# Kernel optimization log

Hardware: AMD Instinct MI355X
Metric: run time of the kernel (lower is better)

Reference implementation:

```python
import jax, jax.numpy as jnp
import numpy as np

MUL = 1024
DIMS = [3, 5, 7, 9]          # irrep dims for l=1,2,3,4
BN_EPS = 1e-5                # e3nn BatchNorm eps
ACT_EPS = 1e-8               # numerical guard for norm-activation sqrt
INV_SQRT_MUL = 1.0 / np.sqrt(MUL)


def bn_act(f, w):
    """e3nn BatchNorm (training mode, component normalization, mean reduce)
    followed by NormActivation(sigmoid, normalize=True).
    f: [B, mul, d] one irrep block; w: [mul] affine batchnorm weight."""
    # norm-based batchnorm: second moment per multiplicity channel
    var = jnp.mean(jnp.mean(f * f, axis=-1), axis=0)            # [mul]
    f = f * ((var + BN_EPS) ** -0.5 * w)[None, :, None]
    # norm-gated sigmoid: out = f * sigmoid(||f||) / ||f||
    n = jnp.sqrt(jnp.sum(f * f, axis=-1, keepdims=True) + ACT_EPS)  # [B, mul, 1]
    return f * (jax.nn.sigmoid(n) / n)


def setup_inputs() -> dict:
    key = jax.random.key(0)
    k = jax.random.split(key, 4)
    B = 1024
    x = jax.random.normal(k[0], (B, 2, 3, 1), dtype=jnp.float32)
    w1 = jax.random.normal(k[1], (2, MUL), dtype=jnp.float32)
    W = jax.random.normal(k[2], (5, 4, MUL, MUL), dtype=jnp.float32)
    bn_w = jnp.ones((6, 4, MUL), dtype=jnp.float32)
    w_out = jax.random.normal(k[3], (MUL, 1), dtype=jnp.float32)
    return {"x": x, "w1": w1, "W": W, "bn_w": bn_w, "w_out": w_out}


def reference(x, w1, W, bn_w, w_out):
    B = x.shape[0]
    x = x.reshape(B, 2, 3)  # '2x1e'
    # block1: only the l=1 path exists; l=2,3,4 outputs are zero
    f1 = jnp.einsum('bui,uv->bvi', x, w1) * (1.0 / jnp.sqrt(2.0).astype(x.dtype))
    fields = [bn_act(f1, bn_w[0, 0])]
    for i, d in enumerate(DIMS[1:]):
        fields.append(bn_act(jnp.zeros((B, MUL, d), x.dtype), bn_w[0, i + 1]))
    # blocks 2..6: per-irrep block linear + norm batchnorm + norm activation
    for b in range(5):
        fields = [
            bn_act(jnp.einsum('bui,uv->bvi', f, W[b, i]) * INV_SQRT_MUL,
                   bn_w[b + 1, i])
            for i, f in enumerate(fields)
        ]
    # out linear: '1024x1e' -> '1x1e'
    out = jnp.einsum('bui,uv->bvi', fields[0], w_out) * INV_SQRT_MUL  # [B,1,3]
    return out.reshape(B, 3)
```

## Files before the change

### kernel.cpp

```cpp
#include <hip/hip_runtime.h>
#include <hip/hip_bf16.h>
#include <cstdint>
#include <cstddef>


typedef short    s16x8 __attribute__((ext_vector_type(8)));
typedef float    f32x4 __attribute__((ext_vector_type(4)));

#define PLANE 1048576

__device__ __forceinline__ unsigned short f2bf(float f) {
  unsigned u = __builtin_bit_cast(unsigned, f);
  u += 0x7FFFu + ((u >> 16) & 1u);
  return (unsigned short)(u >> 16);
}
__device__ __forceinline__ float bf2f(unsigned short h) {
  return __builtin_bit_cast(float, (unsigned)h << 16);
}

__device__ __forceinline__ size_t ablk(int row, int k) {
  return ((size_t)(row >> 6) << 17) + ((size_t)(k >> 5) << 12)
       + ((size_t)((row >> 4) & 3) << 10) + ((size_t)((k >> 3) & 3) << 8)
       + ((size_t)(row & 15) << 4) + ((size_t)(k & 7) << 1);
}

__global__ void convert_w(const float* __restrict__ W,
                          unsigned short* __restrict__ Wh,
                          unsigned short* __restrict__ Wl) {
  __shared__ float t[64][65];
  const int u0 = blockIdx.x * 64, v0 = blockIdx.y * 64;
  const float* Wb = W + (size_t)blockIdx.z * 4194304;
  char* Whb = (char*)(Wh + (size_t)blockIdx.z * PLANE);
  char* Wlb = (char*)(Wl + (size_t)blockIdx.z * PLANE);
  const int c = threadIdx.x & 63, r4 = threadIdx.x >> 6;
#pragma unroll
  for (int i = 0; i < 16; ++i) {
    const int r = i * 4 + r4;
    t[r][c] = Wb[(size_t)(u0 + r) * 1024 + v0 + c];
  }
  __syncthreads();
#pragma unroll
  for (int i = 0; i < 16; ++i) {
    const int r = i * 4 + r4;
    const float w = t[c][r] * 0.03125f;
    const unsigned short hi = f2bf(w);
    const size_t off = ablk(v0 + r, u0 + c);
    *(unsigned short*)(Whb + off) = hi;
    *(unsigned short*)(Wlb + off) = f2bf(w - bf2f(hi));
  }
}

__global__ void layer0_fused(const float* __restrict__ x, const float* __restrict__ w1,
                             float* __restrict__ pre, float* __restrict__ var) {
  const int v = blockIdx.x * 256 + threadIdx.x;
  const int b0 = blockIdx.y * 16;
  const float a0 = w1[v], a1 = w1[1024 + v];
  const float inv = 0.70710678118654752f;
  float ssq = 0.f;
#pragma unroll 4
  for (int bb = 0; bb < 16; ++bb) {
    const int b = b0 + bb;
    const float* xb = x + b * 6;
#pragma unroll
    for (int i = 0; i < 3; ++i) {
      const float f = (xb[i] * a0 + xb[3 + i] * a1) * inv;
      pre[(size_t)i * PLANE + (size_t)b * 1024 + v] = f;
      ssq += f * f;
    }
  }
  atomicAdd(&var[v], ssq);
}

__global__ void act_kernel(const float* __restrict__ pre, const float* __restrict__ var,
                           const float* __restrict__ bnw,
                           char* __restrict__ ah, char* __restrict__ al) {
  const int tid = threadIdx.x;
  const int b  = blockIdx.x * 16 + (tid & 15);
  const int v0 = blockIdx.y * 128 + (tid >> 4) * 8;
  float s[8];
#pragma unroll
  for (int j = 0; j < 8; ++j)
    s[j] = bnw[v0 + j] / sqrtf(var[v0 + j] * (1.0f / 3072.0f) + 1e-5f);
  float f[3][8];
#pragma unroll
  for (int i = 0; i < 3; ++i) {
    const float4 p0 = *(const float4*)&pre[(size_t)i * PLANE + (size_t)b * 1024 + v0];
    const float4 p1 = *(const float4*)&pre[(size_t)i * PLANE + (size_t)b * 1024 + v0 + 4];
    f[i][0] = p0.x * s[0]; f[i][1] = p0.y * s[1]; f[i][2] = p0.z * s[2]; f[i][3] = p0.w * s[3];
    f[i][4] = p1.x * s[4]; f[i][5] = p1.y * s[5]; f[i][6] = p1.z * s[6]; f[i][7] = p1.w * s[7];
  }
#pragma unroll
  for (int j = 0; j < 8; ++j) {
    const float n = sqrtf(f[0][j] * f[0][j] + f[1][j] * f[1][j] + f[2][j] * f[2][j] + 1e-8f);
    const float g = 1.0f / ((1.0f + expf(-n)) * n);
    f[0][j] *= g; f[1][j] *= g; f[2][j] *= g;
  }
#pragma unroll
  for (int i = 0; i < 3; ++i) {
    s16x8 hi, lo;
#pragma unroll
    for (int j = 0; j < 8; ++j) {
      const unsigned short h = f2bf(f[i][j]);
      hi[j] = (short)h;
      lo[j] = (short)f2bf(f[i][j] - bf2f(h));
    }
    const size_t off = ablk(i * 1024 + b, v0);
    *(s16x8*)(ah + off) = hi;
    *(s16x8*)(al + off) = lo;
  }
}

#define LOADF(A_, B_, t_)                                                      \
  {                                                                            \
    const size_t kb_ = (size_t)(t_) << 12;                                     \
    _Pragma("unroll")                                                          \
    for (int m_ = 0; m_ < 4; ++m_) {                                           \
      A_[m_]     = *(const s16x8*)(a_h + kb_ + (m_ << 10));                    \
      A_[4 + m_] = *(const s16x8*)(a_l + kb_ + (m_ << 10));                    \
      B_[m_]     = *(const s16x8*)(b_h + kb_ + (m_ << 10));                    \
      B_[4 + m_] = *(const s16x8*)(b_l + kb_ + (m_ << 10));                    \
    }                                                                          \
  }
#define COMPUTEF(A_, B_)                                                       \
  {                                                                            \
    _Pragma("unroll")                                                          \
    for (int m_ = 0; m_ < 4; ++m_)                                             \
      _Pragma("unroll")                                                        \
      for (int n_ = 0; n_ < 4; ++n_) {                                         \
        acc[m_][n_] = __builtin_amdgcn_mfma_f32_16x16x32_bf16(                 \
            A_[4 + m_], B_[n_], acc[m_][n_], 0, 0, 0);                         \
        acc[m_][n_] = __builtin_amdgcn_mfma_f32_16x16x32_bf16(                 \
            A_[m_], B_[4 + n_], acc[m_][n_], 0, 0, 0);                         \
        acc[m_][n_] = __builtin_amdgcn_mfma_f32_16x16x32_bf16(                 \
            A_[m_], B_[n_], acc[m_][n_], 0, 0, 0);                             \
      }                                                                        \
  }

__global__ __launch_bounds__(128, 2) void gemm_reg(
    const char* __restrict__ Ah, const char* __restrict__ Al,
    const char* __restrict__ Bh, const char* __restrict__ Bl,
    float* __restrict__ C, float* __restrict__ var) {
  __shared__ float red[4096];
  const int bid = blockIdx.x;
  const int xcd = bid & 7, q = bid >> 3;
  const int tm = xcd * 6 + (q % 6);
  const int tn = q / 6;
  const int lane = threadIdx.x & 63;
  const int wave = threadIdx.x >> 6;
  const int rsel = lane & 15, kcsel = lane >> 4;

  const size_t la = ((size_t)lane << 4) + ((size_t)wave << 16);
  const char* a_h = Ah + ((size_t)tm << 17) + la;
  const char* a_l = Al + ((size_t)tm << 17) + la;
  const char* b_h = Bh + ((size_t)tn << 17) + la;
  const char* b_l = Bl + ((size_t)tn << 17) + la;

  f32x4 acc[4][4] = {};
  s16x8 A0[8], B0[8], A1[8], B1[8];

  LOADF(A0, B0, 0);
  LOADF(A1, B1, 1);
  for (int t = 0; t < 14; t += 2) {
    COMPUTEF(A0, B0);
    LOADF(A0, B0, t + 2);
    COMPUTEF(A1, B1);
    LOADF(A1, B1, t + 3);
  }
  COMPUTEF(A0, B0);
  COMPUTEF(A1, B1);

  if (wave == 1) {
#pragma unroll
    for (int m = 0; m < 4; ++m)
#pragma unroll
      for (int n = 0; n < 4; ++n)
#pragma unroll
        for (int j = 0; j < 4; ++j)
          red[(((((m << 2) | n) << 2) | j) << 6) | lane] = acc[m][n][j];
  }
  __syncthreads();
  if (wave == 0) {
    const int r0 = tm * 64 + (kcsel << 2);
    const int c0 = tn * 64 + rsel;
    float csq[4] = {0.f, 0.f, 0.f, 0.f};
#pragma unroll
    for (int m = 0; m < 4; ++m)
#pragma unroll
      for (int n = 0; n < 4; ++n)
#pragma unroll
        for (int j = 0; j < 4; ++j) {
          const float v = acc[m][n][j] + red[(((((m << 2) | n) << 2) | j) << 6) | lane];
          C[(size_t)(r0 + m * 16 + j) * 1024 + c0 + n * 16] = v;
          csq[n] += v * v;
        }
#pragma unroll
    for (int n = 0; n < 4; ++n) {
      csq[n] += __shfl_xor(csq[n], 16);
      csq[n] += __shfl_xor(csq[n], 32);
    }
    if (kcsel == 0) {
#pragma unroll
      for (int n = 0; n < 4; ++n)
        atomicAdd(&var[c0 + n * 16], csq[n]);
    }
  }
}

__global__ void final_kernel(const char* __restrict__ ah, const char* __restrict__ al,
                             const float* __restrict__ wout, float* __restrict__ out) {
  const int b = blockIdx.x, tid = threadIdx.x;
  __shared__ float red[3][4];
  float s[3] = {0.f, 0.f, 0.f};
  if (tid < 128) {
    const int v0 = tid * 8;
#pragma unroll
    for (int i = 0; i < 3; ++i) {
      const size_t off = ablk(i * 1024 + b, v0);
      const s16x8 hi = *(const s16x8*)(ah + off);
      const s16x8 lo = *(const s16x8*)(al + off);
#pragma unroll
      for (int j = 0; j < 8; ++j)
        s[i] += (bf2f((unsigned short)hi[j]) + bf2f((unsigned short)lo[j])) * wout[v0 + j];
    }
  }
#pragma unroll
  for (int i = 0; i < 3; ++i)
    for (int o = 32; o >= 1; o >>= 1) s[i] += __shfl_down(s[i], o);
  if ((tid & 63) == 0)
#pragma unroll
    for (int i = 0; i < 3; ++i) red[i][tid >> 6] = s[i];
  __syncthreads();
  if (tid < 3) {
    const float t = red[tid][0] + red[tid][1] + red[tid][2] + red[tid][3];
    out[b * 3 + tid] = t * 0.03125f;
  }
}

extern "C" void kernel_launch(void* const* d_in, const int* in_sizes, int n_in,
                              void* d_out, int out_size, void* d_ws, size_t ws_size,
                              hipStream_t stream) {
  const float* x    = (const float*)d_in[0];
  const float* w1   = (const float*)d_in[1];
  const float* W    = (const float*)d_in[2];
  const float* bnw  = (const float*)d_in[3];
  const float* wout = (const float*)d_in[4];
  float* out = (float*)d_out;

  char* ws = (char*)d_ws;
  float*          var = (float*)ws;
  float*          pre = (float*)(ws + 32768);
  char*           ah  = ws + 12615680;
  char*           al  = ws + 18907136;
  unsigned short* wh  = (unsigned short*)(ws + 25198592);
  unsigned short* wl  = (unsigned short*)(ws + 35684352);

  hipMemsetAsync(var, 0, 6 * 1024 * sizeof(float), stream);
  convert_w<<<dim3(16, 16, 5), 256, 0, stream>>>(W, wh, wl);
  layer0_fused<<<dim3(4, 64), 256, 0, stream>>>(x, w1, pre, var);
  act_kernel<<<dim3(64, 8), 256, 0, stream>>>(pre, var, bnw, ah, al);
  for (int b = 0; b < 5; ++b) {
    gemm_reg<<<768, 128, 0, stream>>>(
        ah, al, (const char*)(wh + (size_t)b * PLANE), (const char*)(wl + (size_t)b * PLANE),
        pre, var + (b + 1) * 1024);
    act_kernel<<<dim3(64, 8), 256, 0, stream>>>(pre, var + (b + 1) * 1024,
                                                bnw + (size_t)(b + 1) * 4096, ah, al);
  }
  final_kernel<<<1024, 256, 0, stream>>>(ah, al, wout, out);
}
```

Baseline: 195.0 us.

## Compute layer-0 batchnorm analytically from input moments and fuse output projection

Layer 0's per-channel variance is now derived from three second moments of the input (a tiny reduction kernel). This lets the first activation be computed directly from x and w1, with no 12MB pre-activation write and re-read. The final output projection is folded into the last activation kernel using atomicAdd into a zeroed output, removing the final_kernel and the last bf16 split store. The trade-off is an extra single-block kernel, an extra memset, and atomic contention on the output.

```diff
diff --git a/kernel.cpp b/kernel.cpp
--- a/kernel.cpp
+++ b/kernel.cpp
@@ -50,30 +50,80 @@
   }
 }
 
-__global__ void layer0_fused(const float* __restrict__ x, const float* __restrict__ w1,
-                             float* __restrict__ pre, float* __restrict__ var) {
-  const int v = blockIdx.x * 256 + threadIdx.x;
-  const int b0 = blockIdx.y * 16;
-  const float a0 = w1[v], a1 = w1[1024 + v];
-  const float inv = 0.70710678118654752f;
-  float ssq = 0.f;
-#pragma unroll 4
-  for (int bb = 0; bb < 16; ++bb) {
-    const int b = b0 + bb;
+__global__ void xmoments(const float* __restrict__ x, float* __restrict__ M) {
+  float m00 = 0.f, m01 = 0.f, m11 = 0.f;
+  for (int b = threadIdx.x; b < 1024; b += 256) {
     const float* xb = x + b * 6;
 #pragma unroll
     for (int i = 0; i < 3; ++i) {
-      const float f = (xb[i] * a0 + xb[3 + i] * a1) * inv;
-      pre[(size_t)i * PLANE + (size_t)b * 1024 + v] = f;
-      ssq += f * f;
-    }
-  }
-  atomicAdd(&var[v], ssq);
-}
-
+      m00 += xb[i] * xb[i];
+      m01 += xb[i] * xb[3 + i];
+      m11 += xb[3 + i] * xb[3 + i];
+    }
+  }
+  for (int o = 32; o >= 1; o >>= 1) {
+    m00 += __shfl_down(m00, o);
+    m01 += __shfl_down(m01, o);
+    m11 += __shfl_down(m11, o);
+  }
+  __shared__ float r[3][4];
+  if ((threadIdx.x & 63) == 0) {
+    r[0][threadIdx.x >> 6] = m00;
+    r[1][threadIdx.x >> 6] = m01;
+    r[2][threadIdx.x >> 6] = m11;
+  }
+  __syncthreads();
+  if (threadIdx.x < 3)
+    M[threadIdx.x] = (r[threadIdx.x][0] + r[threadIdx.x][1] +
+                      r[threadIdx.x][2] + r[threadIdx.x][3]) * (1.0f / 3072.0f);
+}
+
+__global__ void layer0_act(const float* __restrict__ x, const float* __restrict__ w1,
+                           const float* __restrict__ M, const float* __restrict__ bnw,
+                           char* __restrict__ ah, char* __restrict__ al) {
+  const int tid = threadIdx.x;
+  const int b  = blockIdx.x * 16 + (tid & 15);
+  const int v0 = blockIdx.y * 128 + (tid >> 4) * 8;
+  const float m00 = M[0], m01 = M[1], m11 = M[2];
+  const float* xb = x + b * 6;
+  const float x0[3] = {xb[0], xb[1], xb[2]};
+  const float x1[3] = {xb[3], xb[4], xb[5]};
+  float f[3][8];
+#pragma unroll
+  for (int j = 0; j < 8; ++j) {
+    const float a0 = w1[v0 + j], a1 = w1[1024 + v0 + j];
+    const float varv = 0.5f * (a0 * a0 * m00 + 2.f * a0 * a1 * m01 + a1 * a1 * m11);
+    const float s = bnw[v0 + j] * 0.70710678118654752f / sqrtf(varv + 1e-5f);
+#pragma unroll
+    for (int i = 0; i < 3; ++i)
+      f[i][j] = (x0[i] * a0 + x1[i] * a1) * s;
+  }
+#pragma unroll
+  for (int j = 0; j < 8; ++j) {
+    const float n = sqrtf(f[0][j] * f[0][j] + f[1][j] * f[1][j] + f[2][j] * f[2][j] + 1e-8f);
+    const float g = 1.0f / ((1.0f + expf(-n)) * n);
+    f[0][j] *= g; f[1][j] *= g; f[2][j] *= g;
+  }
+#pragma unroll
+  for (int i = 0; i < 3; ++i) {
+    s16x8 hi, lo;
+#pragma unroll
+    for (int j = 0; j < 8; ++j) {
+      const unsigned short h = f2bf(f[i][j]);
+      hi[j] = (short)h;
+      lo[j] = (short)f2bf(f[i][j] - bf2f(h));
+    }
+    const size_t off = ablk(i * 1024 + b, v0);
+    *(s16x8*)(ah + off) = hi;
+    *(s16x8*)(al + off) = lo;
+  }
+}
+
+template <bool LAST>
 __global__ void act_kernel(const float* __restrict__ pre, const float* __restrict__ var,
                            const float* __restrict__ bnw,
-                           char* __restrict__ ah, char* __restrict__ al) {
+                           char* __restrict__ ah, char* __restrict__ al,
+                           const float* __restrict__ wout, float* __restrict__ out) {
   const int tid = threadIdx.x;
   const int b  = blockIdx.x * 16 + (tid & 15);
   const int v0 = blockIdx.y * 128 + (tid >> 4) * 8;
@@ -95,18 +145,28 @@
     const float g = 1.0f / ((1.0f + expf(-n)) * n);
     f[0][j] *= g; f[1][j] *= g; f[2][j] *= g;
   }
-#pragma unroll
-  for (int i = 0; i < 3; ++i) {
-    s16x8 hi, lo;
-#pragma unroll
-    for (int j = 0; j < 8; ++j) {
-      const unsigned short h = f2bf(f[i][j]);
-      hi[j] = (short)h;
-      lo[j] = (short)f2bf(f[i][j] - bf2f(h));
-    }
-    const size_t off = ablk(i * 1024 + b, v0);
-    *(s16x8*)(ah + off) = hi;
-    *(s16x8*)(al + off) = lo;
+  if (LAST) {
+#pragma unroll
+    for (int i = 0; i < 3; ++i) {
+      float d = 0.f;
+#pragma unroll
+      for (int j = 0; j < 8; ++j) d += f[i][j] * wout[v0 + j];
+      atomicAdd(&out[b * 3 + i], d * 0.03125f);
+    }
+  } else {
+#pragma unroll
+    for (int i = 0; i < 3; ++i) {
+      s16x8 hi, lo;
+#pragma unroll
+      for (int j = 0; j < 8; ++j) {
+        const unsigned short h = f2bf(f[i][j]);
+        hi[j] = (short)h;
+        lo[j] = (short)f2bf(f[i][j] - bf2f(h));
+      }
+      const size_t off = ablk(i * 1024 + b, v0);
+      *(s16x8*)(ah + off) = hi;
+      *(s16x8*)(al + off) = lo;
+    }
   }
 }
 
@@ -206,36 +266,6 @@
   }
 }
 
-__global__ void final_kernel(const char* __restrict__ ah, const char* __restrict__ al,
-                             const float* __restrict__ wout, float* __restrict__ out) {
-  const int b = blockIdx.x, tid = threadIdx.x;
-  __shared__ float red[3][4];
-  float s[3] = {0.f, 0.f, 0.f};
-  if (tid < 128) {
-    const int v0 = tid * 8;
-#pragma unroll
-    for (int i = 0; i < 3; ++i) {
-      const size_t off = ablk(i * 1024 + b, v0);
-      const s16x8 hi = *(const s16x8*)(ah + off);
-      const s16x8 lo = *(const s16x8*)(al + off);
-#pragma unroll
-      for (int j = 0; j < 8; ++j)
-        s[i] += (bf2f((unsigned short)hi[j]) + bf2f((unsigned short)lo[j])) * wout[v0 + j];
-    }
-  }
-#pragma unroll
-  for (int i = 0; i < 3; ++i)
-    for (int o = 32; o >= 1; o >>= 1) s[i] += __shfl_down(s[i], o);
-  if ((tid & 63) == 0)
-#pragma unroll
-    for (int i = 0; i < 3; ++i) red[i][tid >> 6] = s[i];
-  __syncthreads();
-  if (tid < 3) {
-    const float t = red[tid][0] + red[tid][1] + red[tid][2] + red[tid][3];
-    out[b * 3 + tid] = t * 0.03125f;
-  }
-}
-
 extern "C" void kernel_launch(void* const* d_in, const int* in_sizes, int n_in,
                               void* d_out, int out_size, void* d_ws, size_t ws_size,
                               hipStream_t stream) {
@@ -248,6 +278,7 @@
 
   char* ws = (char*)d_ws;
   float*          var = (float*)ws;
+  float*          Mb  = (float*)(ws + 24576);
   float*          pre = (float*)(ws + 32768);
   char*           ah  = ws + 12615680;
   char*           al  = ws + 18907136;
@@ -255,15 +286,21 @@
   unsigned short* wl  = (unsigned short*)(ws + 35684352);
 
   hipMemsetAsync(var, 0, 6 * 1024 * sizeof(float), stream);
+  hipMemsetAsync(out, 0, (size_t)out_size * sizeof(float), stream);
   convert_w<<<dim3(16, 16, 5), 256, 0, stream>>>(W, wh, wl);
-  layer0_fused<<<dim3(4, 64), 256, 0, stream>>>(x, w1, pre, var);
-  act_kernel<<<dim3(64, 8), 256, 0, stream>>>(pre, var, bnw, ah, al);
+  xmoments<<<1, 256, 0, stream>>>(x, Mb);
+  layer0_act<<<dim3(64, 8), 256, 0, stream>>>(x, w1, Mb, bnw, ah, al);
   for (int b = 0; b < 5; ++b) {
     gemm_reg<<<768, 128, 0, stream>>>(
         ah, al, (const char*)(wh + (size_t)b * PLANE), (const char*)(wl + (size_t)b * PLANE),
         pre, var + (b + 1) * 1024);
-    act_kernel<<<dim3(64, 8), 256, 0, stream>>>(pre, var + (b + 1) * 1024,
-                                                bnw + (size_t)(b + 1) * 4096, ah, al);
-  }
-  final_kernel<<<1024, 256, 0, stream>>>(ah, al, wout, out);
-}
+    if (b < 4)
+      act_kernel<false><<<dim3(64, 8), 256, 0, stream>>>(
+          pre, var + (b + 1) * 1024, bnw + (size_t)(b + 1) * 4096,
+          ah, al, nullptr, nullptr);
+    else
+      act_kernel<true><<<dim3(64, 8), 256, 0, stream>>>(
+          pre, var + 5 * 1024, bnw + (size_t)5 * 4096,
+          ah, al, wout, out);
+  }
+}
```

Result: no change. 193.9 us (-0.6%).
